# Kernel optimization log

Measured on AMD Instinct MI355X. Metric: run time of the kernel, lower is better.

Reference implementation:

```python
import jax, jax.numpy as jnp
import numpy as np
from math import sqrt


def _build_transitions(dim):
    # Upper-triangular (i<=j) pairs in the same row-major order as the torch loop.
    iu0, iu1 = np.triu_indices(dim)
    n_mono = len(iu0)
    idx = np.arange(n_mono)
    M = np.zeros((dim, dim), dtype=np.int32)
    M[iu0, iu1] = idx
    M[iu1, iu0] = idx
    coef_trans = np.full((n_mono, 1), sqrt(2.0), dtype=np.float32)
    coef_trans[idx[iu0 == iu1]] = 1.0  # diagonal coefficients stay scale 1
    return iu0, iu1, M.reshape(-1), coef_trans


def setup_inputs() -> dict:
    key = jax.random.key(0)
    k1, k2, k3, k4 = jax.random.split(key, 4)
    dim, n_quadrics, B = 512, 64, 2048
    n_mono = dim * (dim - 1) // 2 + dim  # 131328
    points = jax.random.normal(k1, (B, dim), dtype=jnp.float32)
    # orthogonal-ish init is only an init detail; random normal keeps math identical
    q_coefs = jax.random.normal(k2, (n_mono, n_quadrics), dtype=jnp.float32) / np.sqrt(n_mono)
    l_coefs = 2.0 * jax.random.uniform(k3, (dim, n_quadrics), dtype=jnp.float32) - 1.0
    free_coefs = 2.0 * jax.random.uniform(k4, (1, n_quadrics), dtype=jnp.float32) - 1.0
    return {"points": points, "q_coefs": q_coefs, "l_coefs": l_coefs, "free_coefs": free_coefs}


def reference(points, q_coefs, l_coefs, free_coefs):
    B, dim = points.shape
    nq = q_coefs.shape[1]
    iu0, iu1, inds_trans, coef_trans_np = _build_transitions(dim)
    coef_trans = jnp.asarray(coef_trans_np)

    # quadratic monomials: q[b, k] = p[b, i_k] * p[b, j_k]  (upper-tri order)
    q = points[:, iu0] * points[:, iu1]  # (B, n_mono)

    coefs = q_coefs * coef_trans  # (n_mono, nq) real coefficients

    # values of quadrics at points
    values = jnp.abs(q @ coefs + points @ l_coefs + free_coefs)  # (B, nq)

    # symmetric full matrices gathered from flat coefficient vector
    m_full = coefs[inds_trans].reshape(dim, dim, nq)  # (dim, dim, nq)
    dm = (jnp.eye(dim, dtype=points.dtype) + 1.0)[:, :, None]  # 2 on diag, ... wait: eye+ones -> 2 diag, 1 off
    m_scaled = m_full * dm

    # gradients: grad[b, k, e] = sum_d p[b, d] * m_scaled[d, e, k] + l_coefs[e, k]
    q_grad = jnp.einsum("bd,dek->bke", points, m_scaled) + l_coefs.T[None, :, :]  # (B, nq, dim)
    grad = jnp.sum(q_grad * q_grad, axis=2)  # (B, nq)

    norm = jnp.linalg.norm(q_coefs, axis=0)  # (nq,)
    scores = (jnp.sqrt(grad / 4.0 + values * norm) - jnp.sqrt(grad) / 2.0) / norm
    return scores
```

## Files before the change

### kernel.cpp

```cpp
#include <hip/hip_runtime.h>

#define DIM 512
#define NQ 64
#define BATCH 2048

typedef __bf16  bf16x8  __attribute__((ext_vector_type(8)));
typedef float   floatx4 __attribute__((ext_vector_type(4)));

static __device__ inline unsigned short f2bf(float f) {
    unsigned int u = __float_as_uint(f);
    return (unsigned short)((u + 0x7fffu + ((u >> 16) & 1u)) >> 16);
}
static __device__ inline float bf2f(unsigned short h) {
    return __uint_as_float((unsigned int)h << 16);
}
static __device__ inline unsigned int pack2(float a, float b) {
    return (unsigned)f2bf(a) | ((unsigned)f2bf(b) << 16);
}

__global__ void hsq_pack_kernel(const float* __restrict__ pts,
                                unsigned short* __restrict__ Pb) {
    const int i8 = blockIdx.x * 256 + threadIdx.x;
    const float4 v1 = *(const float4*)(pts + (size_t)i8 * 8);
    const float4 v2 = *(const float4*)(pts + (size_t)i8 * 8 + 4);
    uint4 wv;
    wv.x = pack2(v1.x, v1.y); wv.y = pack2(v1.z, v1.w);
    wv.z = pack2(v2.x, v2.y); wv.w = pack2(v2.z, v2.w);
    *(uint4*)(Pb + (size_t)i8 * 8) = wv;
}

__global__ __launch_bounds__(256, 4)
void hsq_expand_kernel(const float* __restrict__ qc,
                       unsigned short* __restrict__ W,
                       float* __restrict__ npart) {
    const int e    = blockIdx.x;
    const int dblk = blockIdx.y;
    const int pb   = blockIdx.y * 512 + blockIdx.x;
    const int wid  = threadIdx.x >> 6;
    const int k    = threadIdx.x & 63;
    const int d0   = dblk * 128 + wid * 32;

    __shared__ unsigned short tv[64 * 136];
    __shared__ float part[4][64];

    float v[32];
#pragma unroll
    for (int s = 0; s < 32; ++s) {
        const int d = d0 + s;
        const int i = d < e ? d : e;
        const int j = d < e ? e : d;
        const int idx = i * DIM - ((i * (i - 1)) >> 1) + (j - i);
        v[s] = qc[(size_t)idx * NQ + k];
    }

    float nacc = 0.0f;
#pragma unroll
    for (int s = 0; s < 32; ++s)
        if (d0 + s >= e) nacc += v[s] * v[s];

#pragma unroll
    for (int t = 0; t < 4; ++t) {
        float sc[8];
#pragma unroll
        for (int q = 0; q < 8; ++q) {
            const int d = d0 + t * 8 + q;
            sc[q] = v[t * 8 + q] * ((d == e) ? 2.0f : 1.41421356237309515f);
        }
        uint4 w;
        w.x = pack2(sc[0], sc[1]); w.y = pack2(sc[2], sc[3]);
        w.z = pack2(sc[4], sc[5]); w.w = pack2(sc[6], sc[7]);
        *(uint4*)&tv[k * 136 + wid * 32 + t * 8] = w;
    }
    part[wid][k] = nacc;
    __syncthreads();

#pragma unroll
    for (int r = 0; r < 4; ++r) {
        const int kk = r * 16 + (threadIdx.x >> 4);
        const int u  = threadIdx.x & 15;
        const uint4 w = *(const uint4*)&tv[kk * 136 + u * 8];
        *(uint4*)(W + ((size_t)(kk * DIM + e)) * DIM + dblk * 128 + u * 8) = w;
    }
    if (threadIdx.x < 64) {
        npart[(size_t)k * 2048 + pb] =
            part[0][k] + part[1][k] + part[2][k] + part[3][k];
    }
}

__global__ __launch_bounds__(256, 3)
void hsq_gemm_kernel(const unsigned short* __restrict__ Pb,
                     const unsigned short* __restrict__ W,
                     const float* __restrict__ l_coefs,
                     float2* __restrict__ part) {
    const int bid = blockIdx.x;
    const int xcd = bid & 7;
    const int loc = bid >> 3;
    const int k   = xcd * 8 + (loc >> 6);
    const int rem = loc & 63;
    const int eb  = rem >> 4;
    const int m0  = (rem & 15) * 128;

    const int tid   = threadIdx.x;
    const int w     = tid >> 6;
    const int lane  = tid & 63;
    const int mhalf = w >> 1, nhalf = w & 1;
    const int c     = lane & 15;
    const int quad  = lane >> 4;

    __shared__ unsigned short Ab[2][128 * 32];
    __shared__ unsigned short Bb[2][128 * 32];
    __shared__ float red[2][128][2];

    const unsigned short* Wk = W + (size_t)k * DIM * DIM + (size_t)eb * 128 * DIM;

#define STAGE(buf_, it_) do {                                                   \
    const int lr_  = lane >> 2;                                                 \
    const int gch_ = (lane & 3) ^ ((lane >> 3) & 3);                            \
    _Pragma("unroll")                                                           \
    for (int i_ = 0; i_ < 2; ++i_) {                                            \
        const int rb_  = w * 32 + i_ * 16;                                      \
        const int row_ = rb_ + lr_;                                             \
        __builtin_amdgcn_global_load_lds(                                       \
            (const __attribute__((address_space(1))) unsigned int*)             \
                (Pb + (size_t)(m0 + row_) * DIM + (it_) * 32 + gch_ * 8),       \
            (__attribute__((address_space(3))) unsigned int*)                   \
                &Ab[buf_][rb_ * 32], 16, 0, 0);                                 \
        __builtin_amdgcn_global_load_lds(                                       \
            (const __attribute__((address_space(1))) unsigned int*)             \
                (Wk + (size_t)row_ * DIM + (it_) * 32 + gch_ * 8),              \
            (__attribute__((address_space(3))) unsigned int*)                   \
                &Bb[buf_][rb_ * 32], 16, 0, 0);                                 \
    }                                                                           \
} while (0)

    floatx4 acc[4][4];
#pragma unroll
    for (int mt = 0; mt < 4; ++mt)
#pragma unroll
        for (int nt = 0; nt < 4; ++nt)
            acc[mt][nt] = (floatx4){0.f, 0.f, 0.f, 0.f};

    STAGE(0, 0);
    __syncthreads();

    for (int it = 0; it < 16; ++it) {
        const int buf = it & 1;
        if (it < 15) STAGE(buf ^ 1, it + 1);

        bf16x8 af[4], bfr[4];
#pragma unroll
        for (int mt = 0; mt < 4; ++mt) {
            const int row  = mhalf * 64 + mt * 16 + c;
            const int slot = quad ^ ((row >> 1) & 3);
            af[mt] = *(const bf16x8*)&Ab[buf][row * 32 + slot * 8];
        }
#pragma unroll
        for (int nt = 0; nt < 4; ++nt) {
            const int er   = nhalf * 64 + nt * 16 + c;
            const int slot = quad ^ ((er >> 1) & 3);
            bfr[nt] = *(const bf16x8*)&Bb[buf][er * 32 + slot * 8];
        }
#pragma unroll
        for (int mt = 0; mt < 4; ++mt)
#pragma unroll
            for (int nt = 0; nt < 4; ++nt)
                acc[mt][nt] = __builtin_amdgcn_mfma_f32_16x16x32_bf16(
                    af[mt], bfr[nt], acc[mt][nt], 0, 0, 0);
        __syncthreads();
    }
#undef STAGE

    float lcv[4];
#pragma unroll
    for (int nt = 0; nt < 4; ++nt)
        lcv[nt] = l_coefs[(eb * 128 + nhalf * 64 + nt * 16 + c) * NQ + k];

    const unsigned short* Pe = Pb + (size_t)(m0 + mhalf * 64) * DIM
                                  + eb * 128 + nhalf * 64 + c;
#pragma unroll
    for (int mt = 0; mt < 4; ++mt)
#pragma unroll
        for (int r = 0; r < 4; ++r) {
            const unsigned short* Prow = Pe + (size_t)(mt * 16 + quad * 4 + r) * DIM;
            float pv = 0.f, pg = 0.f;
#pragma unroll
            for (int nt = 0; nt < 4; ++nt) {
                const float g = acc[mt][nt][r];
                const float l = lcv[nt];
                pv += bf2f(Prow[nt * 16]) * (0.5f * g + l);
                const float gq = g + l;
                pg += gq * gq;
            }
#pragma unroll
            for (int off = 1; off < 16; off <<= 1) {
                pv += __shfl_xor(pv, off);
                pg += __shfl_xor(pg, off);
            }
            if (c == 0) {
                const int row = mhalf * 64 + mt * 16 + quad * 4 + r;
                red[nhalf][row][0] = pv;
                red[nhalf][row][1] = pg;
            }
        }
    __syncthreads();

    if (tid < 128) {
        const float pv = red[0][tid][0] + red[1][tid][0];
        const float pg = red[0][tid][1] + red[1][tid][1];
        part[((size_t)(eb * NQ + k)) * BATCH + m0 + tid] = make_float2(pv, pg);
    }
}

__global__ void hsq_final_kernel(const float2* __restrict__ part,
                                 const float* __restrict__ npart,
                                 const float* __restrict__ free_coefs,
                                 float* __restrict__ out) {
    const int k = blockIdx.x;
    const int t = threadIdx.x;
    __shared__ float ws[4];

    const float4* src = (const float4*)(npart + (size_t)k * 2048);
    const float4 a = src[t * 2], b = src[t * 2 + 1];
    float s = a.x + a.y + a.z + a.w + b.x + b.y + b.z + b.w;
#pragma unroll
    for (int off = 1; off < 64; off <<= 1) s += __shfl_xor(s, off);
    if ((t & 63) == 0) ws[t >> 6] = s;
    __syncthreads();
    const float nrm = sqrtf(ws[0] + ws[1] + ws[2] + ws[3]);
    const float fc  = free_coefs[k];

#pragma unroll
    for (int i = 0; i < 8; ++i) {
        const int bidx = i * 256 + t;
        float pv = 0.f, pg = 0.f;
#pragma unroll
        for (int eb = 0; eb < 4; ++eb) {
            const float2 p = part[((size_t)(eb * NQ + k)) * BATCH + bidx];
            pv += p.x; pg += p.y;
        }
        const float vals = fabsf(pv + fc);
        out[(size_t)bidx * NQ + k] = (sqrtf(0.25f * pg + vals * nrm) - 0.5f * sqrtf(pg)) / nrm;
    }
}

extern "C" void kernel_launch(void* const* d_in, const int* in_sizes, int n_in,
                              void* d_out, int out_size, void* d_ws, size_t ws_size,
                              hipStream_t stream) {
    const float* points     = (const float*)d_in[0];
    const float* q_coefs    = (const float*)d_in[1];
    const float* l_coefs    = (const float*)d_in[2];
    const float* free_coefs = (const float*)d_in[3];
    float* out = (float*)d_out;

    char* ws = (char*)d_ws;
    unsigned short* W  = (unsigned short*)ws;
    unsigned short* Pb = (unsigned short*)(ws + 33554432);
    float2*         part  = (float2*)(ws + 35651584);
    float*          npart = (float*)(ws + 39845888);

    hsq_pack_kernel<<<dim3(BATCH * DIM / 8 / 256), 256, 0, stream>>>(points, Pb);
    hsq_expand_kernel<<<dim3(DIM, 4), 256, 0, stream>>>(q_coefs, W, npart);
    hsq_gemm_kernel<<<dim3(NQ * 64), 256, 0, stream>>>(Pb, W, l_coefs, part);
    hsq_final_kernel<<<dim3(NQ), 256, 0, stream>>>(part, npart, free_coefs, out);
}
```

Baseline: 205.7 us.

## Enlarge GEMM tiles to 256x256 with 8 waves and phased LDS pipeline

Restructures the batched GEMM to use 256x256 output tiles per 512-thread workgroup with 128 KB dynamic LDS, staging 64-wide K slices in half-tiles interleaved with MFMA phases. Each phase is separated by barriers and raises wave priority during MFMA. The larger tiles are meant to cut redundant global loads of Pb and W and raise arithmetic intensity per LDS load. The cost is higher register pressure (8x4 accumulators), lower occupancy, and a smaller grid of 1024 blocks, with the final kernel reducing over 2 e-tiles instead of 4.

```diff
diff --git a/kernel.cpp b/kernel.cpp
--- a/kernel.cpp
+++ b/kernel.cpp
@@ -87,107 +87,156 @@
     }
 }
 
-__global__ __launch_bounds__(256, 3)
+__global__ __launch_bounds__(512, 2)
 void hsq_gemm_kernel(const unsigned short* __restrict__ Pb,
                      const unsigned short* __restrict__ W,
                      const float* __restrict__ l_coefs,
                      float2* __restrict__ part) {
+    extern __shared__ unsigned short smem[];
+
     const int bid = blockIdx.x;
-    const int xcd = bid & 7;
-    const int loc = bid >> 3;
-    const int k   = xcd * 8 + (loc >> 6);
-    const int rem = loc & 63;
-    const int eb  = rem >> 4;
-    const int m0  = (rem & 15) * 128;
-
-    const int tid   = threadIdx.x;
-    const int w     = tid >> 6;
-    const int lane  = tid & 63;
-    const int mhalf = w >> 1, nhalf = w & 1;
-    const int c     = lane & 15;
-    const int quad  = lane >> 4;
-
-    __shared__ unsigned short Ab[2][128 * 32];
-    __shared__ unsigned short Bb[2][128 * 32];
-    __shared__ float red[2][128][2];
-
-    const unsigned short* Wk = W + (size_t)k * DIM * DIM + (size_t)eb * 128 * DIM;
-
-#define STAGE(buf_, it_) do {                                                   \
-    const int lr_  = lane >> 2;                                                 \
-    const int gch_ = (lane & 3) ^ ((lane >> 3) & 3);                            \
-    _Pragma("unroll")                                                           \
-    for (int i_ = 0; i_ < 2; ++i_) {                                            \
-        const int rb_  = w * 32 + i_ * 16;                                      \
-        const int row_ = rb_ + lr_;                                             \
-        __builtin_amdgcn_global_load_lds(                                       \
-            (const __attribute__((address_space(1))) unsigned int*)             \
-                (Pb + (size_t)(m0 + row_) * DIM + (it_) * 32 + gch_ * 8),       \
-            (__attribute__((address_space(3))) unsigned int*)                   \
-                &Ab[buf_][rb_ * 32], 16, 0, 0);                                 \
-        __builtin_amdgcn_global_load_lds(                                       \
-            (const __attribute__((address_space(1))) unsigned int*)             \
-                (Wk + (size_t)row_ * DIM + (it_) * 32 + gch_ * 8),              \
-            (__attribute__((address_space(3))) unsigned int*)                   \
-                &Bb[buf_][rb_ * 32], 16, 0, 0);                                 \
-    }                                                                           \
+    const int wg  = (bid & 7) * 128 + (bid >> 3);
+    const int k   = wg >> 4;
+    const int rem = wg & 15;
+    const int et  = rem >> 3;
+    const int mt  = rem & 7;
+    const int m0  = mt * 256;
+
+    const int tid  = threadIdx.x;
+    const int lane = tid & 63;
+    const int w    = tid >> 6;
+    const int wm   = w >> 2;
+    const int wn   = w & 3;
+    const int c    = lane & 15;
+    const int quad = lane >> 4;
+
+    const unsigned short* Wk = W + ((size_t)k * DIM + (size_t)et * 256) * DIM;
+
+    const int scolb = ((tid & 7) * 16) ^ (((tid >> 3) & 7) << 4);
+    const unsigned short* pAs = Pb + (size_t)(m0 + (tid >> 3)) * DIM + (scolb >> 1);
+    const unsigned short* pBs = Wk + (size_t)(tid >> 3) * DIM + (scolb >> 1);
+
+    const int xorv  = (c & 7) << 4;
+    const int koff0 = ((0 * 64 + quad * 16) ^ xorv) >> 1;
+    const int koff1 = ((1 * 64 + quad * 16) ^ xorv) >> 1;
+    const int awoff = wm * 8192 + c * 64;
+    const int bwoff = (wn >> 1) * 8192 + (wn & 1) * 4096 + c * 64;
+
+#define STAGE_HALF(LDSELEM, GSRC) do {                                         \
+    _Pragma("unroll")                                                          \
+    for (int cc_ = 0; cc_ < 2; ++cc_) {                                        \
+        __builtin_amdgcn_global_load_lds(                                      \
+            (const __attribute__((address_space(1))) unsigned int*)            \
+                ((GSRC) + (size_t)(cc_ * 64) * DIM),                           \
+            (__attribute__((address_space(3))) unsigned int*)                  \
+                (smem + (LDSELEM) + cc_ * 4096 + tid * 8),                     \
+            16, 0, 0);                                                         \
+    }                                                                          \
 } while (0)
 
-    floatx4 acc[4][4];
-#pragma unroll
-    for (int mt = 0; mt < 4; ++mt)
-#pragma unroll
-        for (int nt = 0; nt < 4; ++nt)
-            acc[mt][nt] = (floatx4){0.f, 0.f, 0.f, 0.f};
-
-    STAGE(0, 0);
+#define LOADB(BBASE) do {                                                      \
+    _Pragma("unroll")                                                          \
+    for (int ni_ = 0; ni_ < 4; ++ni_) {                                        \
+        bfr[ni_][0] = *(const bf16x8*)(smem + (BBASE) + bwoff + ni_ * 1024 + koff0); \
+        bfr[ni_][1] = *(const bf16x8*)(smem + (BBASE) + bwoff + ni_ * 1024 + koff1); \
+    }                                                                          \
+} while (0)
+
+#define PHASE(ABASE, MI0, PRE_B, STAGE_AND_WAIT) do {                          \
+    bf16x8 a00 = *(const bf16x8*)(smem + (ABASE) + awoff + (MI0) * 1024 + koff0);     \
+    bf16x8 a01 = *(const bf16x8*)(smem + (ABASE) + awoff + (MI0) * 1024 + koff1);     \
+    bf16x8 a10 = *(const bf16x8*)(smem + (ABASE) + awoff + ((MI0) + 1) * 1024 + koff0); \
+    bf16x8 a11 = *(const bf16x8*)(smem + (ABASE) + awoff + ((MI0) + 1) * 1024 + koff1); \
+    PRE_B;                                                                     \
+    STAGE_AND_WAIT;                                                            \
+    asm volatile("" ::: "memory");                                             \
+    __builtin_amdgcn_s_barrier();                                              \
+    asm volatile("" ::: "memory");                                             \
+    __builtin_amdgcn_s_setprio(1);                                             \
+    _Pragma("unroll")                                                          \
+    for (int ni_ = 0; ni_ < 4; ++ni_) {                                        \
+        acc[(MI0)][ni_]     = __builtin_amdgcn_mfma_f32_16x16x32_bf16(a00, bfr[ni_][0], acc[(MI0)][ni_], 0, 0, 0);     \
+        acc[(MI0)][ni_]     = __builtin_amdgcn_mfma_f32_16x16x32_bf16(a01, bfr[ni_][1], acc[(MI0)][ni_], 0, 0, 0);     \
+        acc[(MI0) + 1][ni_] = __builtin_amdgcn_mfma_f32_16x16x32_bf16(a10, bfr[ni_][0], acc[(MI0) + 1][ni_], 0, 0, 0); \
+        acc[(MI0) + 1][ni_] = __builtin_amdgcn_mfma_f32_16x16x32_bf16(a11, bfr[ni_][1], acc[(MI0) + 1][ni_], 0, 0, 0); \
+    }                                                                          \
+    __builtin_amdgcn_s_setprio(0);                                             \
+    asm volatile("" ::: "memory");                                             \
+    __builtin_amdgcn_s_barrier();                                              \
+    asm volatile("" ::: "memory");                                             \
+} while (0)
+
+    floatx4 acc[8][4];
+#pragma unroll
+    for (int mi = 0; mi < 8; ++mi)
+#pragma unroll
+        for (int ni = 0; ni < 4; ++ni)
+            acc[mi][ni] = (floatx4){0.f, 0.f, 0.f, 0.f};
+
+    bf16x8 bfr[4][2];
+
+    STAGE_HALF(0,             pAs);
+    STAGE_HALF(8192,          pAs + 128 * DIM);
+    STAGE_HALF(16384,         pBs);
+    STAGE_HALF(16384 + 8192,  pBs + 128 * DIM);
+    STAGE_HALF(49152,         pBs + 64);
+    STAGE_HALF(49152 + 8192,  pBs + 128 * DIM + 64);
+    asm volatile("s_waitcnt vmcnt(4)" ::: "memory");
+    __builtin_amdgcn_s_barrier();
+    asm volatile("" ::: "memory");
+
+    for (int it = 0; it < 4; ++it) {
+        const unsigned short* pA1 = pAs + (size_t)(2 * it + 1) * 64;
+        const unsigned short* pB2 = pBs + (size_t)(2 * it + 2) * 64;
+        const unsigned short* pA2 = pAs + (size_t)(2 * it + 2) * 64;
+        const unsigned short* pB3 = pBs + (size_t)(2 * it + 3) * 64;
+
+        PHASE(0, 0, LOADB(16384), { STAGE_HALF(32768, pA1); });
+        PHASE(0, 2, ((void)0),    { STAGE_HALF(32768 + 8192, pA1 + 128 * DIM); });
+        PHASE(0, 4, ((void)0),    { if (it < 3) STAGE_HALF(16384, pB2); });
+        PHASE(0, 6, ((void)0), {
+            if (it < 3) {
+                STAGE_HALF(16384 + 8192, pB2 + 128 * DIM);
+                asm volatile("s_waitcnt vmcnt(4)" ::: "memory");
+            } else {
+                asm volatile("s_waitcnt vmcnt(0)" ::: "memory");
+            }
+        });
+        PHASE(32768, 0, LOADB(49152), { if (it < 3) STAGE_HALF(0, pA2); });
+        PHASE(32768, 2, ((void)0),    { if (it < 3) STAGE_HALF(8192, pA2 + 128 * DIM); });
+        PHASE(32768, 4, ((void)0),    { if (it < 3) STAGE_HALF(49152, pB3); });
+        PHASE(32768, 6, ((void)0), {
+            if (it < 3) {
+                STAGE_HALF(49152 + 8192, pB3 + 128 * DIM);
+                asm volatile("s_waitcnt vmcnt(4)" ::: "memory");
+            }
+        });
+    }
+#undef PHASE
+#undef LOADB
+#undef STAGE_HALF
+
     __syncthreads();
 
-    for (int it = 0; it < 16; ++it) {
-        const int buf = it & 1;
-        if (it < 15) STAGE(buf ^ 1, it + 1);
-
-        bf16x8 af[4], bfr[4];
-#pragma unroll
-        for (int mt = 0; mt < 4; ++mt) {
-            const int row  = mhalf * 64 + mt * 16 + c;
-            const int slot = quad ^ ((row >> 1) & 3);
-            af[mt] = *(const bf16x8*)&Ab[buf][row * 32 + slot * 8];
-        }
-#pragma unroll
-        for (int nt = 0; nt < 4; ++nt) {
-            const int er   = nhalf * 64 + nt * 16 + c;
-            const int slot = quad ^ ((er >> 1) & 3);
-            bfr[nt] = *(const bf16x8*)&Bb[buf][er * 32 + slot * 8];
-        }
-#pragma unroll
-        for (int mt = 0; mt < 4; ++mt)
-#pragma unroll
-            for (int nt = 0; nt < 4; ++nt)
-                acc[mt][nt] = __builtin_amdgcn_mfma_f32_16x16x32_bf16(
-                    af[mt], bfr[nt], acc[mt][nt], 0, 0, 0);
-        __syncthreads();
-    }
-#undef STAGE
-
     float lcv[4];
 #pragma unroll
-    for (int nt = 0; nt < 4; ++nt)
-        lcv[nt] = l_coefs[(eb * 128 + nhalf * 64 + nt * 16 + c) * NQ + k];
-
-    const unsigned short* Pe = Pb + (size_t)(m0 + mhalf * 64) * DIM
-                                  + eb * 128 + nhalf * 64 + c;
-#pragma unroll
-    for (int mt = 0; mt < 4; ++mt)
+    for (int ni = 0; ni < 4; ++ni)
+        lcv[ni] = l_coefs[(et * 256 + wn * 64 + ni * 16 + c) * NQ + k];
+
+    const unsigned short* Pe = Pb + (size_t)(m0 + wm * 128) * DIM + et * 256 + wn * 64 + c;
+    float* red = (float*)smem;
+
+#pragma unroll
+    for (int mi = 0; mi < 8; ++mi)
 #pragma unroll
         for (int r = 0; r < 4; ++r) {
-            const unsigned short* Prow = Pe + (size_t)(mt * 16 + quad * 4 + r) * DIM;
+            const unsigned short* Prow = Pe + (size_t)(mi * 16 + quad * 4 + r) * DIM;
             float pv = 0.f, pg = 0.f;
 #pragma unroll
-            for (int nt = 0; nt < 4; ++nt) {
-                const float g = acc[mt][nt][r];
-                const float l = lcv[nt];
-                pv += bf2f(Prow[nt * 16]) * (0.5f * g + l);
+            for (int ni = 0; ni < 4; ++ni) {
+                const float g = acc[mi][ni][r];
+                const float l = lcv[ni];
+                pv += bf2f(Prow[ni * 16]) * (0.5f * g + l);
                 const float gq = g + l;
                 pg += gq * gq;
             }
@@ -197,17 +246,25 @@
                 pg += __shfl_xor(pg, off);
             }
             if (c == 0) {
-                const int row = mhalf * 64 + mt * 16 + quad * 4 + r;
-                red[nhalf][row][0] = pv;
-                red[nhalf][row][1] = pg;
+                const int row16 = mi * 16 + quad * 4 + r;
+                red[(w * 128 + row16) * 2 + 0] = pv;
+                red[(w * 128 + row16) * 2 + 1] = pg;
             }
         }
     __syncthreads();
 
-    if (tid < 128) {
-        const float pv = red[0][tid][0] + red[1][tid][0];
-        const float pg = red[0][tid][1] + red[1][tid][1];
-        part[((size_t)(eb * NQ + k)) * BATCH + m0 + tid] = make_float2(pv, pg);
+    if (tid < 256) {
+        const int row16 = tid & 127;
+        const int wmf   = tid >> 7;
+        float pv = 0.f, pg = 0.f;
+#pragma unroll
+        for (int wnf = 0; wnf < 4; ++wnf) {
+            const int wi = wmf * 4 + wnf;
+            pv += red[(wi * 128 + row16) * 2 + 0];
+            pg += red[(wi * 128 + row16) * 2 + 1];
+        }
+        part[((size_t)(et * NQ + k)) * BATCH + m0 + wmf * 128 + row16] =
+            make_float2(pv, pg);
     }
 }
 
@@ -234,7 +291,7 @@
         const int bidx = i * 256 + t;
         float pv = 0.f, pg = 0.f;
 #pragma unroll
-        for (int eb = 0; eb < 4; ++eb) {
+        for (int eb = 0; eb < 2; ++eb) {
             const float2 p = part[((size_t)(eb * NQ + k)) * BATCH + bidx];
             pv += p.x; pg += p.y;
         }
@@ -256,10 +313,18 @@
     unsigned short* W  = (unsigned short*)ws;
     unsigned short* Pb = (unsigned short*)(ws + 33554432);
     float2*         part  = (float2*)(ws + 35651584);
-    float*          npart = (float*)(ws + 39845888);
+    float*          npart = (float*)(ws + 37748736);
+
+    static bool attr_done = false;
+    if (!attr_done) {
+        (void)hipFuncSetAttribute((const void*)hsq_gemm_kernel,
+                                  hipFuncAttributeMaxDynamicSharedMemorySize,
+                                  131072);
+        attr_done = true;
+    }
 
     hsq_pack_kernel<<<dim3(BATCH * DIM / 8 / 256), 256, 0, stream>>>(points, Pb);
     hsq_expand_kernel<<<dim3(DIM, 4), 256, 0, stream>>>(q_coefs, W, npart);
-    hsq_gemm_kernel<<<dim3(NQ * 64), 256, 0, stream>>>(Pb, W, l_coefs, part);
+    hsq_gemm_kernel<<<dim3(1024), dim3(512), 131072, stream>>>(Pb, W, l_coefs, part);
     hsq_final_kernel<<<dim3(NQ), 256, 0, stream>>>(part, npart, free_coefs, out);
 }
```

After: 194.3 us. 1.06x faster.
